# Optimization experiments

Measured on AMD Instinct MI355X. Metric: run time of the kernel, lower is better.

## Reference

```python
import jax, jax.numpy as jnp
import numpy as np

D = 768
H0, H1 = 1536, 768  # mlp_layers '1536,768'


def setup_inputs() -> dict:
    key = jax.random.key(0)
    ks = jax.random.split(key, 8)
    bsz, C, l_x, l_y = 8, 64, 256, 256
    xs = jax.random.normal(ks[0], (bsz, l_x, D), dtype=jnp.float32)
    ys = jax.random.normal(ks[1], (bsz, C, l_y, D), dtype=jnp.float32)
    # torch.nn.Linear weights: [out_features, in_features]
    def lin(k, fout, fin):
        bound = 1.0 / np.sqrt(fin)
        kw, kb = jax.random.split(k)
        W = jax.random.uniform(kw, (fout, fin), jnp.float32, -bound, bound)
        b = jax.random.uniform(kb, (fout,), jnp.float32, -bound, bound)
        return W, b
    W0, b0 = lin(ks[2], H0, 2 * D)
    W1, b1 = lin(ks[3], H1, H0)
    W2, b2 = lin(ks[4], 1, H1)
    return {"xs": xs, "ys": ys, "W0": W0, "b0": b0, "W1": W1, "b1": b1, "W2": W2, "b2": b2}


def reference(xs, ys, W0, b0, W1, b1, W2, b2):
    bsz, l_x, d = xs.shape
    _, C, l_y, _ = ys.shape
    # dot-product scores: [bsz, C, l_x, l_y]
    scores = jnp.einsum('bxd,bcyd->bcxy', xs, ys)
    argmax_idx = jnp.argmax(scores, axis=-1)  # [bsz, C, l_x]
    # gather winning y vector for each x token: [bsz, C, l_x, d]
    idx = jnp.broadcast_to(argmax_idx[..., None], (bsz, C, l_x, d))
    y_sel = jnp.take_along_axis(ys, idx, axis=2)
    xs_exp = jnp.broadcast_to(xs[:, None], (bsz, C, l_x, d))
    # stack then flatten(start_dim=-2) == concat along last dim: [bsz,C,l_x,2d]
    h = jnp.concatenate([xs_exp, y_sel], axis=-1)
    # MLP (dropout is identity at inference)
    h = jax.nn.softplus(jnp.einsum('bcxi,oi->bcxo', h, W0) + b0)
    h = jax.nn.softplus(jnp.einsum('bcxi,oi->bcxo', h, W1) + b1)
    s = jnp.einsum('bcxi,oi->bcxo', h, W2) + b2  # [bsz,C,l_x,1]
    return jnp.sum(s[..., 0], axis=-1)  # [bsz, C]
```

## Files before the change

### kernel.cpp

```cpp
#include <hip/hip_runtime.h>
#include <stdint.h>

#define DB   8
#define DC   64
#define DLX  256
#define DLY  256
#define DD   768
#define DH0  1536
#define DH1  768
#define NBC  (DB*DC)
#define NTOK (NBC*DLX)
#define TAU  0.25f

typedef float f32x4 __attribute__((ext_vector_type(4)));
typedef _Float16 f16x8 __attribute__((ext_vector_type(8)));
typedef _Float16 f16x4 __attribute__((ext_vector_type(4)));

__device__ __forceinline__ float softplusf(float x){
  float t = __builtin_amdgcn_exp2f(-fabsf(x) * 1.44269504f);
  return fmaxf(x, 0.0f) + 0.69314718f * __builtin_amdgcn_logf(1.0f + t);
}

__device__ __forceinline__ void gload_lds16(const void* g, void* l){
  __builtin_amdgcn_global_load_lds((const __attribute__((address_space(1))) void*)g,
                                   (__attribute__((address_space(3))) void*)l,
                                   16, 0, 0);
}

__global__ __launch_bounds__(256) void k_cvt16(const float* __restrict__ src, int ld, int off,
                                               int rows, int cols, _Float16* __restrict__ dst){
  int total = rows * (cols >> 3);
  for (int idx = blockIdx.x * 256 + threadIdx.x; idx < total; idx += gridDim.x * 256){
    int r = idx / (cols >> 3), c8 = (idx % (cols >> 3)) * 8;
    const float* s = src + (size_t)r * ld + off + c8;
    float4 f0 = *(const float4*)s, f1 = *(const float4*)(s + 4);
    f16x8 v;
    v[0]=(_Float16)f0.x; v[1]=(_Float16)f0.y; v[2]=(_Float16)f0.z; v[3]=(_Float16)f0.w;
    v[4]=(_Float16)f1.x; v[5]=(_Float16)f1.y; v[6]=(_Float16)f1.z; v[7]=(_Float16)f1.w;
    *(f16x8*)(dst + (size_t)r * cols + c8) = v;
  }
}

__global__ __launch_bounds__(1024, 2) void k_scores4(const _Float16* __restrict__ xs16,
                                                     const float* __restrict__ ys,
                                                     const float* __restrict__ xs,
                                                     _Float16* __restrict__ ys16,
                                                     int* __restrict__ widx){
  const int bc = blockIdx.x, b = bc >> 6;
  const float* Y = ys + (size_t)bc * DLY * DD;
  __shared__ __align__(16) _Float16 As[256 * 32];
  __shared__ __align__(16) _Float16 Bs[256 * 32];
  __shared__ float rmx[256][4];
  __shared__ float gm[256];
  __shared__ unsigned short cand[256][8];
  __shared__ int ccnt[256];
  const int tid = threadIdx.x;
  const int l = tid & 63, w = tid >> 6;
  const int wr = w >> 2, wc = w & 3;
  const int lrow = l & 15, lg = l >> 4;
  const int kq = (lg ^ (lrow & 3)) * 8;
  const int kg = (((l & 3) ^ ((l >> 2) & 3))) * 8;
  const _Float16* srcA = xs16 + ((size_t)b * DLX + w*16 + (l >> 2)) * DD + kg;
  const int r = tid >> 2, c8 = (tid & 3) * 8;
  const float* srcB = Y + (size_t)r * DD + c8;
  _Float16* ydst = ys16 + ((size_t)bc * DLY + r) * DD + c8;
  const int bslot = (((tid & 3) ^ (r & 3))) * 8;

  f32x4 acc[4][4];
  #pragma unroll
  for (int i = 0; i < 4; i++)
    #pragma unroll
    for (int j = 0; j < 4; j++) acc[i][j] = (f32x4){0.f,0.f,0.f,0.f};

  for (int k0 = 0; k0 < DD; k0 += 32){
    float4 f0 = *(const float4*)(srcB + k0);
    float4 f1 = *(const float4*)(srcB + k0 + 4);
    f16x8 hv;
    hv[0]=(_Float16)f0.x; hv[1]=(_Float16)f0.y; hv[2]=(_Float16)f0.z; hv[3]=(_Float16)f0.w;
    hv[4]=(_Float16)f1.x; hv[5]=(_Float16)f1.y; hv[6]=(_Float16)f1.z; hv[7]=(_Float16)f1.w;
    __syncthreads();
    gload_lds16(srcA + k0, As + w*512);
    *(f16x8*)&Bs[r*32 + bslot] = hv;
    *(f16x8*)(ydst + k0) = hv;
    __syncthreads();
    f16x8 af[4], bf[4];
    #pragma unroll
    for (int i = 0; i < 4; i++){
      af[i] = *(const f16x8*)&As[(wr*64 + i*16 + lrow)*32 + kq];
      bf[i] = *(const f16x8*)&Bs[(wc*64 + i*16 + lrow)*32 + kq];
    }
    #pragma unroll
    for (int i = 0; i < 4; i++)
      #pragma unroll
      for (int j = 0; j < 4; j++)
        acc[i][j] = __builtin_amdgcn_mfma_f32_16x16x32_f16(af[i], bf[j], acc[i][j], 0, 0, 0);
  }

  #pragma unroll
  for (int i = 0; i < 4; i++)
    #pragma unroll
    for (int r2 = 0; r2 < 4; r2++){
      float m = fmaxf(fmaxf(acc[i][0][r2], acc[i][1][r2]), fmaxf(acc[i][2][r2], acc[i][3][r2]));
      m = fmaxf(m, __shfl_xor(m, 1));
      m = fmaxf(m, __shfl_xor(m, 2));
      m = fmaxf(m, __shfl_xor(m, 4));
      m = fmaxf(m, __shfl_xor(m, 8));
      if (lrow == 0) rmx[wr*64 + i*16 + lg*4 + r2][wc] = m;
    }
  __syncthreads();
  if (tid < 256){
    gm[tid] = fmaxf(fmaxf(rmx[tid][0], rmx[tid][1]), fmaxf(rmx[tid][2], rmx[tid][3]));
    ccnt[tid] = 0;
  }
  __syncthreads();
  #pragma unroll
  for (int i = 0; i < 4; i++)
    #pragma unroll
    for (int r2 = 0; r2 < 4; r2++){
      int t = wr*64 + i*16 + lg*4 + r2;
      float thr = gm[t] - TAU;
      #pragma unroll
      for (int j = 0; j < 4; j++){
        float s = acc[i][j][r2];
        if (s >= thr){
          int p = atomicAdd(&ccnt[t], 1);
          if (p < 8) cand[t][p] = (unsigned short)(wc*64 + j*16 + lrow);
        }
      }
    }
  __syncthreads();
  for (int it = 0; it < 16; it++){
    int t = w * 16 + it;
    int cnt = ccnt[t];
    int by;
    if (cnt == 1){
      by = cand[t][0];
    } else {
      const float* xr = xs + ((size_t)b * DLX + t) * DD;
      float best = -1e30f; int besty = 0;
      int n = (cnt <= 8) ? cnt : 256;
      for (int p = 0; p < n; p++){
        int c = (cnt <= 8) ? (int)cand[t][p] : p;
        const float* yr = Y + (size_t)c * DD;
        float s = 0.f;
        #pragma unroll
        for (int q = 0; q < 3; q++){
          float4 xv = *(const float4*)(xr + l*12 + q*4);
          float4 yv = *(const float4*)(yr + l*12 + q*4);
          s += xv.x*yv.x + xv.y*yv.y + xv.z*yv.z + xv.w*yv.w;
        }
        s += __shfl_xor(s, 1);  s += __shfl_xor(s, 2);  s += __shfl_xor(s, 4);
        s += __shfl_xor(s, 8);  s += __shfl_xor(s, 16); s += __shfl_xor(s, 32);
        if (s > best || (s == best && c < besty)){ best = s; besty = c; }
      }
      by = besty;
    }
    if (l == 0) widx[(size_t)bc * DLX + t] = by;
  }
}

template<int MODE>
__global__ __launch_bounds__(512) void k_gemm16(const _Float16* __restrict__ A,
        unsigned bdelta,
        const int* __restrict__ widx,
        const _Float16* __restrict__ X0h,
        const float* __restrict__ bias,
        const float* __restrict__ w2,
        float* __restrict__ outF,
        _Float16* __restrict__ outH){
  constexpr int K = (MODE == 2) ? DH0 : DD;
  __shared__ __align__(16) _Float16 As[128 * 64];
  __shared__ __align__(16) _Float16 Bs[256 * 64];
  const int tid = threadIdx.x;
  const int gx = gridDim.x, nwg = gx * gridDim.y;
  int lin = blockIdx.x + gx * blockIdx.y;
  int swz = (lin & 7) * (nwg >> 3) + (lin >> 3);
  const int n0  = (swz % gx) * 256;
  const int by  = swz / gx;
  const int rt0 = by * 128;
  const int l = tid & 63, w = tid >> 6;
  const int wr = w >> 2, wc = w & 3;
  const int lrow = l & 15, lg = l >> 4;

  int bc = 0, xb = 0, b = 0;
  if constexpr (MODE == 1){ bc = by >> 1; xb = (by & 1) * 128; b = bc >> 6; }

  const int urow = l >> 3;
  const int uslot = (l & 7) ^ (urow & 7);
  unsigned goff[6];
  _Float16* ldst[6];
  #pragma unroll
  for (int i = 0; i < 6; i++){
    int u = w*6 + i;
    if (u < 16){
      int row = u*8 + urow;
      unsigned aoff;
      if constexpr (MODE == 1){
        int yi = widx[bc * DLX + xb + row];
        aoff = (unsigned)((bc * DLY + yi) * DD);
      } else {
        aoff = (unsigned)((rt0 + row) * K);
      }
      goff[i] = aoff + uslot*8;
      ldst[i] = (_Float16*)As + u*512;
    } else {
      int row = (u - 16)*8 + urow;
      goff[i] = bdelta + (unsigned)((n0 + row) * K) + uslot*8;
      ldst[i] = (_Float16*)Bs + (u - 16)*512;
    }
  }

  f32x4 acc[4][4];
  #pragma unroll
  for (int i = 0; i < 4; i++)
    #pragma unroll
    for (int j = 0; j < 4; j++) acc[i][j] = (f32x4){0.f,0.f,0.f,0.f};

  for (int k0 = 0; k0 < K; k0 += 64){
    __syncthreads();
    #pragma unroll
    for (int i = 0; i < 6; i++)
      gload_lds16(A + (size_t)(goff[i] + (unsigned)k0), ldst[i]);
    __syncthreads();
    #pragma unroll
    for (int kh = 0; kh < 2; kh++){
      const int rc = ((kh*4 + lg) ^ (lrow & 7)) * 8;
      f16x8 af[4], bf[4];
      #pragma unroll
      for (int i = 0; i < 4; i++){
        af[i] = *(const f16x8*)&As[(wr*64 + i*16 + lrow)*64 + rc];
        bf[i] = *(const f16x8*)&Bs[(wc*64 + i*16 + lrow)*64 + rc];
      }
      #pragma unroll
      for (int i = 0; i < 4; i++)
        #pragma unroll
        for (int j = 0; j < 4; j++)
          acc[i][j] = __builtin_amdgcn_mfma_f32_16x16x32_f16(af[i], bf[j], acc[i][j], 0, 0, 0);
    }
  }

  if constexpr (MODE == 0){
    #pragma unroll
    for (int mi = 0; mi < 4; mi++)
      #pragma unroll
      for (int ni = 0; ni < 4; ni++){
        int n = n0 + wc*64 + ni*16 + lrow;
        float bv = bias[n];
        #pragma unroll
        for (int r = 0; r < 4; r++){
          int m = wr*64 + mi*16 + lg*4 + r;
          outH[(size_t)(rt0 + m) * DH0 + n] = (_Float16)(acc[mi][ni][r] + bv);
        }
      }
  } else if constexpr (MODE == 1){
    #pragma unroll
    for (int mi = 0; mi < 4; mi++)
      #pragma unroll
      for (int ni = 0; ni < 4; ni++){
        int n = n0 + wc*64 + ni*16 + lrow;
        #pragma unroll
        for (int r = 0; r < 4; r++){
          int m = wr*64 + mi*16 + lg*4 + r;
          float x0v = (float)X0h[((size_t)b * DLX + xb + m) * DH0 + n];
          float v = softplusf(acc[mi][ni][r] + x0v);
          outH[(size_t)(rt0 + m) * DH0 + n] = (_Float16)v;
        }
      }
  } else {
    float p[4][4];
    #pragma unroll
    for (int mi = 0; mi < 4; mi++)
      #pragma unroll
      for (int r = 0; r < 4; r++) p[mi][r] = 0.f;
    #pragma unroll
    for (int ni = 0; ni < 4; ni++){
      int n = n0 + wc*64 + ni*16 + lrow;
      float b1v = bias[n], w2v = w2[n];
      #pragma unroll
      for (int mi = 0; mi < 4; mi++)
        #pragma unroll
        for (int r = 0; r < 4; r++)
          p[mi][r] += softplusf(acc[mi][ni][r] + b1v) * w2v;
    }
    const int nb = (int)(swz % gx);
    #pragma unroll
    for (int mi = 0; mi < 4; mi++)
      #pragma unroll
      for (int r = 0; r < 4; r++){
        float s = p[mi][r];
        s += __shfl_xor(s, 1);
        s += __shfl_xor(s, 2);
        s += __shfl_xor(s, 4);
        s += __shfl_xor(s, 8);
        if (lrow == 0){
          size_t t = (size_t)rt0 + wr*64 + mi*16 + lg*4 + r;
          outF[t * 12 + nb*4 + wc] = s;
        }
      }
  }
}

__global__ __launch_bounds__(256) void k_reduce(const float* __restrict__ spart,
                                                const float* __restrict__ b2,
                                                float* __restrict__ out){
  int bc = blockIdx.x, tid = threadIdx.x;
  const float* p = spart + ((size_t)bc * DLX + tid) * 12;
  float s = 0.0f;
  #pragma unroll
  for (int j = 0; j < 12; j++) s += p[j];
  __shared__ float red[256];
  red[tid] = s;
  __syncthreads();
  for (int off = 128; off > 0; off >>= 1){
    if (tid < off) red[tid] += red[tid + off];
    __syncthreads();
  }
  if (tid == 0) out[bc] = red[0] + 256.0f * b2[0];
}

extern "C" void kernel_launch(void* const* d_in, const int* in_sizes, int n_in,
                              void* d_out, int out_size, void* d_ws, size_t ws_size,
                              hipStream_t stream){
  const float* xs = (const float*)d_in[0];
  const float* ys = (const float*)d_in[1];
  const float* W0 = (const float*)d_in[2];
  const float* b0 = (const float*)d_in[3];
  const float* W1 = (const float*)d_in[4];
  const float* b1 = (const float*)d_in[5];
  const float* W2 = (const float*)d_in[6];
  const float* b2 = (const float*)d_in[7];
  float* out = (float*)d_out;

  char* wsp = (char*)d_ws;
  size_t off = 0;
  auto alloc = [&](size_t bytes)->void*{
    void* p = wsp + off;
    off += (bytes + 255) & ~(size_t)255;
    return p;
  };
  int* widx        = (int*)alloc((size_t)NTOK * 4);
  _Float16* ys16   = (_Float16*)alloc((size_t)NBC * DLY * DD * 2);
  _Float16* W0yf   = (_Float16*)alloc((size_t)DH0 * DD * 2);
  _Float16* xs16   = (_Float16*)alloc((size_t)DB * DLX * DD * 2);
  _Float16* W0xf   = (_Float16*)alloc((size_t)DH0 * DD * 2);
  _Float16* X0h    = (_Float16*)alloc((size_t)DB * DLX * DH0 * 2);
  float* spart     = (float*)alloc((size_t)NTOK * 12 * 4);
  _Float16* H0     = (_Float16*)alloc((size_t)NTOK * DH0 * 2);
  _Float16* W1f    = (_Float16*)alloc((size_t)DH1 * DH0 * 2);

  unsigned d0 = (unsigned)(W0xf - xs16);
  unsigned d1 = (unsigned)(W0yf - ys16);
  unsigned d2 = (unsigned)(W1f - H0);

  k_cvt16<<<dim3(576),  256, 0, stream>>>(W0, DH0, 0,  DH0, DD, W0xf);
  k_cvt16<<<dim3(576),  256, 0, stream>>>(W0, DH0, DD, DH0, DD, W0yf);
  k_cvt16<<<dim3(576),  256, 0, stream>>>(W1, DH0, 0,  DH1, DH0, W1f);
  k_cvt16<<<dim3(768),  256, 0, stream>>>(xs, DD, 0, DB*DLX, DD, xs16);
  k_scores4<<<dim3(NBC), 1024, 0, stream>>>(xs16, ys, xs, ys16, widx);
  k_gemm16<0><<<dim3(6, 16),   512, 0, stream>>>(xs16, d0, nullptr, nullptr, b0, nullptr, nullptr, X0h);
  k_gemm16<1><<<dim3(6, 1024), 512, 0, stream>>>(ys16, d1, widx, X0h, nullptr, nullptr, nullptr, H0);
  k_gemm16<2><<<dim3(3, 1024), 512, 0, stream>>>(H0, d2, nullptr, nullptr, b1, W2, spart, nullptr);
  k_reduce<<<NBC, 256, 0, stream>>>(spart, b2, out);
}
```

Measured before the change: 921.4 us.

## Triple-buffer LDS tiles with async global-to-LDS prefetch in fp16 GEMM

```diff
diff --git a/kernel.cpp b/kernel.cpp
--- a/kernel.cpp
+++ b/kernel.cpp
@@ -169,8 +169,9 @@
         float* __restrict__ outF,
         _Float16* __restrict__ outH){
   constexpr int K = (MODE == 2) ? DH0 : DD;
-  __shared__ __align__(16) _Float16 As[128 * 64];
-  __shared__ __align__(16) _Float16 Bs[256 * 64];
+  constexpr int NT = K / 32;
+  constexpr unsigned BUFH = 12288;
+  __shared__ __align__(16) _Float16 S[3 * BUFH];
   const int tid = threadIdx.x;
   const int gx = gridDim.x, nwg = gx * gridDim.y;
   int lin = blockIdx.x + gx * blockIdx.y;
@@ -181,19 +182,20 @@
   const int l = tid & 63, w = tid >> 6;
   const int wr = w >> 2, wc = w & 3;
   const int lrow = l & 15, lg = l >> 4;
+  const int kq = (lg ^ (lrow & 3)) * 8;
 
   int bc = 0, xb = 0, b = 0;
   if constexpr (MODE == 1){ bc = by >> 1; xb = (by & 1) * 128; b = bc >> 6; }
 
-  const int urow = l >> 3;
-  const int uslot = (l & 7) ^ (urow & 7);
-  unsigned goff[6];
-  _Float16* ldst[6];
-  #pragma unroll
-  for (int i = 0; i < 6; i++){
-    int u = w*6 + i;
-    if (u < 16){
-      int row = u*8 + urow;
+  const int urow = l >> 2;
+  const int kg = (((l & 3) ^ (urow & 3))) * 8;
+  unsigned goff[3];
+  unsigned ldoff[3];
+  #pragma unroll
+  for (int i = 0; i < 3; i++){
+    int u = w*3 + i;
+    if (u < 8){
+      int row = u*16 + urow;
       unsigned aoff;
       if constexpr (MODE == 1){
         int yi = widx[bc * DLX + xb + row];
@@ -201,12 +203,12 @@
       } else {
         aoff = (unsigned)((rt0 + row) * K);
       }
-      goff[i] = aoff + uslot*8;
-      ldst[i] = (_Float16*)As + u*512;
+      goff[i] = aoff + kg;
+      ldoff[i] = u * 512;
     } else {
-      int row = (u - 16)*8 + urow;
-      goff[i] = bdelta + (unsigned)((n0 + row) * K) + uslot*8;
-      ldst[i] = (_Float16*)Bs + (u - 16)*512;
+      int row = (u - 8)*16 + urow;
+      goff[i] = bdelta + (unsigned)((n0 + row) * K) + kg;
+      ldoff[i] = 4096 + (u - 8) * 512;
     }
   }
 
@@ -216,27 +218,36 @@
     #pragma unroll
     for (int j = 0; j < 4; j++) acc[i][j] = (f32x4){0.f,0.f,0.f,0.f};
 
-  for (int k0 = 0; k0 < K; k0 += 64){
-    __syncthreads();
-    #pragma unroll
-    for (int i = 0; i < 6; i++)
-      gload_lds16(A + (size_t)(goff[i] + (unsigned)k0), ldst[i]);
-    __syncthreads();
-    #pragma unroll
-    for (int kh = 0; kh < 2; kh++){
-      const int rc = ((kh*4 + lg) ^ (lrow & 7)) * 8;
-      f16x8 af[4], bf[4];
-      #pragma unroll
-      for (int i = 0; i < 4; i++){
-        af[i] = *(const f16x8*)&As[(wr*64 + i*16 + lrow)*64 + rc];
-        bf[i] = *(const f16x8*)&Bs[(wc*64 + i*16 + lrow)*64 + rc];
-      }
-      #pragma unroll
-      for (int i = 0; i < 4; i++)
-        #pragma unroll
-        for (int j = 0; j < 4; j++)
-          acc[i][j] = __builtin_amdgcn_mfma_f32_16x16x32_f16(af[i], bf[j], acc[i][j], 0, 0, 0);
-    }
+  #pragma unroll
+  for (int i = 0; i < 3; i++) gload_lds16(A + (size_t)goff[i], &S[ldoff[i]]);
+  #pragma unroll
+  for (int i = 0; i < 3; i++) gload_lds16(A + (size_t)(goff[i] + 32u), &S[BUFH + ldoff[i]]);
+
+  unsigned oc = 0, on = BUFH, os = 2*BUFH;
+  for (int T = 0; T < NT; T++){
+    if (T + 2 < NT){
+      #pragma unroll
+      for (int i = 0; i < 3; i++)
+        gload_lds16(A + (size_t)(goff[i] + (unsigned)((T+2)*32)), &S[os + ldoff[i]]);
+      asm volatile("s_waitcnt vmcnt(3)" ::: "memory");
+    } else {
+      asm volatile("s_waitcnt vmcnt(0)" ::: "memory");
+    }
+    __builtin_amdgcn_s_barrier();
+    const _Float16* Sb = &S[oc];
+    f16x8 af[4], bf[4];
+    #pragma unroll
+    for (int i = 0; i < 4; i++){
+      af[i] = *(const f16x8*)&Sb[(wr*64 + i*16 + lrow)*32 + kq];
+      bf[i] = *(const f16x8*)&Sb[4096 + (wc*64 + i*16 + lrow)*32 + kq];
+    }
+    #pragma unroll
+    for (int i = 0; i < 4; i++)
+      #pragma unroll
+      for (int j = 0; j < 4; j++)
+        acc[i][j] = __builtin_amdgcn_mfma_f32_16x16x32_f16(af[i], bf[j], acc[i][j], 0, 0, 0);
+    __builtin_amdgcn_s_barrier();
+    unsigned t = oc; oc = on; on = os; os = t;
   }
 
   if constexpr (MODE == 0){
```

Result: slower. 953.7 us (+3.5%).
